# Optimization experiments

Measured on AMD Instinct MI355X. Metric: run time of the kernel, lower is better.

## Reference

```python
import jax, jax.numpy as jnp
import numpy as np
from jax import lax


def _viterbi_decode(logits, trans):
    """Batched Viterbi decode (tf.contrib.crf.crf_decode semantics, full lengths).
    logits: [B, T, U] unary potentials; trans: [U, U], trans[i, j] = score(i -> j).
    Returns int32 tags [B, T]."""
    logits_t = jnp.swapaxes(logits, 0, 1)  # [T, B, U]
    init_v = logits_t[0]                   # [B, U]

    def fwd_step(v, logit_t):
        # scores[b, i, j] = v[b, i] + trans[i, j]
        scores = v[:, :, None] + trans[None, :, :]          # [B, U, U]
        bp = jnp.argmax(scores, axis=1).astype(jnp.int32)   # [B, U] best prev tag
        v_new = jnp.max(scores, axis=1) + logit_t           # [B, U]
        return v_new, bp

    v_last, bps = lax.scan(fwd_step, init_v, logits_t[1:])  # bps: [T-1, B, U]
    last_tag = jnp.argmax(v_last, axis=1).astype(jnp.int32)  # [B]

    def bwd_step(tag, bp):
        # tag is the tag at t+1; bp[b, k] = best tag at t given tag k at t+1
        new_tag = jnp.take_along_axis(bp, tag[:, None], axis=1)[:, 0]
        return new_tag, new_tag

    _, tags_prefix = lax.scan(bwd_step, last_tag, bps, reverse=True)  # [T-1, B]
    tags = jnp.concatenate([tags_prefix, last_tag[None, :]], axis=0)  # [T, B]
    return jnp.swapaxes(tags, 0, 1)  # [B, T]


def setup_inputs() -> dict:
    key = jax.random.key(0)
    k0, k1, k2, k3, k4 = jax.random.split(key, 5)
    B, T, D, U = 64, 512, 1024, 128
    x = jax.random.normal(k0, (B, T, D), dtype=jnp.float32)
    kernel = jax.random.normal(k1, (D, U), dtype=jnp.float32) * (1.0 / np.sqrt(D))
    bias = jnp.zeros((U,), dtype=jnp.float32)
    chain_kernel = jax.random.normal(k2, (U, U), dtype=jnp.float32) * 0.1
    left_boundary = jax.random.normal(k3, (U,), dtype=jnp.float32) * 0.1
    right_boundary = jax.random.normal(k4, (U,), dtype=jnp.float32) * 0.1
    return {
        "x": x,
        "kernel": kernel,
        "bias": bias,
        "chain_kernel": chain_kernel,
        "left_boundary": left_boundary,
        "right_boundary": right_boundary,
    }


def reference(x, kernel, bias, chain_kernel, left_boundary, right_boundary):
    # _dense_layer: linear activation, x @ kernel + bias
    logits = jnp.einsum("btd,du->btu", x, kernel) + bias  # [B, T, U]
    # add_boundary_energy with mask=None: boundaries on first / last timestep
    logits = logits.at[:, 0, :].add(left_boundary)
    logits = logits.at[:, -1, :].add(right_boundary)
    # test_mode='viterbi', learn_mode='join': return decoded tags cast to float32
    tags = _viterbi_decode(logits, chain_kernel)
    return tags.astype(jnp.float32)
```

## Files before the change

kernel.cpp:

```cpp
#include <hip/hip_runtime.h>

#define T_SEQ 512
#define U_TAGS 128
#define D_DIM 1024
#define M_ROWS (64 * T_SEQ)

__global__ __launch_bounds__(256) void crf_gemm_half(
    const float* __restrict__ A, const float* __restrict__ Bk,
    float* __restrict__ Cpart) {
  __shared__ float As[16][132];
  __shared__ float Bs[16][132];
  const int tid = threadIdx.x;
  const int tx = tid & 15, ty = tid >> 4;
  const int row0 = blockIdx.x * 128;
  const int kbase = blockIdx.y * (D_DIM / 2);

  const int am = tid >> 2, ak = (tid & 3) << 2;
  const int bk = tid >> 5, bn = (tid & 31) << 2;

  float acc[8][8] = {};

  float4 a0 = *(const float4*)&A[(size_t)(row0 + am) * D_DIM + kbase + ak];
  float4 a1 = *(const float4*)&A[(size_t)(row0 + am + 64) * D_DIM + kbase + ak];
  float4 b0 = *(const float4*)&Bk[(size_t)(kbase + bk) * U_TAGS + bn];
  float4 b1 = *(const float4*)&Bk[(size_t)(kbase + bk + 8) * U_TAGS + bn];

  for (int k0 = 0; k0 < D_DIM / 2; k0 += 16) {
    As[ak + 0][am] = a0.x; As[ak + 1][am] = a0.y;
    As[ak + 2][am] = a0.z; As[ak + 3][am] = a0.w;
    As[ak + 0][am + 64] = a1.x; As[ak + 1][am + 64] = a1.y;
    As[ak + 2][am + 64] = a1.z; As[ak + 3][am + 64] = a1.w;
    *(float4*)&Bs[bk][bn] = b0;
    *(float4*)&Bs[bk + 8][bn] = b1;
    __syncthreads();
    if (k0 + 16 < D_DIM / 2) {
      const int kn = kbase + k0 + 16;
      a0 = *(const float4*)&A[(size_t)(row0 + am) * D_DIM + kn + ak];
      a1 = *(const float4*)&A[(size_t)(row0 + am + 64) * D_DIM + kn + ak];
      b0 = *(const float4*)&Bk[(size_t)(kn + bk) * U_TAGS + bn];
      b1 = *(const float4*)&Bk[(size_t)(kn + bk + 8) * U_TAGS + bn];
    }
#pragma unroll
    for (int kk = 0; kk < 16; ++kk) {
      float a[8], b[8];
      *(float4*)&a[0] = *(const float4*)&As[kk][ty * 8];
      *(float4*)&a[4] = *(const float4*)&As[kk][ty * 8 + 4];
      *(float4*)&b[0] = *(const float4*)&Bs[kk][tx * 4];
      *(float4*)&b[4] = *(const float4*)&Bs[kk][tx * 4 + 64];
#pragma unroll
      for (int r = 0; r < 8; ++r)
#pragma unroll
        for (int c = 0; c < 8; ++c) acc[r][c] = fmaf(a[r], b[c], acc[r][c]);
    }
    __syncthreads();
  }

  float* Cp = Cpart + (size_t)blockIdx.y * M_ROWS * U_TAGS;
#pragma unroll
  for (int r = 0; r < 8; ++r) {
    const int row = row0 + ty * 8 + r;
    *(float4*)&Cp[(size_t)row * U_TAGS + tx * 4] = *(float4*)&acc[r][0];
    *(float4*)&Cp[(size_t)row * U_TAGS + tx * 4 + 64] = *(float4*)&acc[r][4];
  }
}

__global__ __launch_bounds__(256) void crf_combine(
    float* __restrict__ p, const float* __restrict__ bias,
    const float* __restrict__ lb, const float* __restrict__ rb) {
  const int i = blockIdx.x * 256 + threadIdx.x;
  const int row = i >> 5;
  const int col = (i & 31) << 2;
  const int t = row & (T_SEQ - 1);
  const float* p1 = p + (size_t)M_ROWS * U_TAGS;
  float4 v0 = *(const float4*)&p[(size_t)i * 4];
  float4 v1 = *(const float4*)&p1[(size_t)i * 4];
  float4 bb = *(const float4*)&bias[col];
  float4 o;
  o.x = v0.x + v1.x + bb.x; o.y = v0.y + v1.y + bb.y;
  o.z = v0.z + v1.z + bb.z; o.w = v0.w + v1.w + bb.w;
  if (t == 0) {
    float4 l = *(const float4*)&lb[col];
    o.x += l.x; o.y += l.y; o.z += l.z; o.w += l.w;
  }
  if (t == T_SEQ - 1) {
    float4 r = *(const float4*)&rb[col];
    o.x += r.x; o.y += r.y; o.z += r.z; o.w += r.w;
  }
  *(float4*)&p[(size_t)i * 4] = o;
}

__global__ __launch_bounds__(256) void crf_gemm(
    const float* __restrict__ A, const float* __restrict__ Bk,
    const float* __restrict__ bias, const float* __restrict__ lb,
    const float* __restrict__ rb, float* __restrict__ C) {
  __shared__ float As[16][132];
  __shared__ float Bs[16][132];
  const int tid = threadIdx.x;
  const int tx = tid & 15, ty = tid >> 4;
  const int row0 = blockIdx.x * 128;
  const int am = tid >> 2, ak = (tid & 3) << 2;
  const int bk = tid >> 5, bn = (tid & 31) << 2;
  float acc[8][8] = {};
  float4 a0 = *(const float4*)&A[(size_t)(row0 + am) * D_DIM + ak];
  float4 a1 = *(const float4*)&A[(size_t)(row0 + am + 64) * D_DIM + ak];
  float4 b0 = *(const float4*)&Bk[(size_t)bk * U_TAGS + bn];
  float4 b1 = *(const float4*)&Bk[(size_t)(bk + 8) * U_TAGS + bn];
  for (int k0 = 0; k0 < D_DIM; k0 += 16) {
    As[ak + 0][am] = a0.x; As[ak + 1][am] = a0.y;
    As[ak + 2][am] = a0.z; As[ak + 3][am] = a0.w;
    As[ak + 0][am + 64] = a1.x; As[ak + 1][am + 64] = a1.y;
    As[ak + 2][am + 64] = a1.z; As[ak + 3][am + 64] = a1.w;
    *(float4*)&Bs[bk][bn] = b0;
    *(float4*)&Bs[bk + 8][bn] = b1;
    __syncthreads();
    if (k0 + 16 < D_DIM) {
      a0 = *(const float4*)&A[(size_t)(row0 + am) * D_DIM + k0 + 16 + ak];
      a1 = *(const float4*)&A[(size_t)(row0 + am + 64) * D_DIM + k0 + 16 + ak];
      b0 = *(const float4*)&Bk[(size_t)(k0 + 16 + bk) * U_TAGS + bn];
      b1 = *(const float4*)&Bk[(size_t)(k0 + 16 + bk + 8) * U_TAGS + bn];
    }
#pragma unroll
    for (int kk = 0; kk < 16; ++kk) {
      float a[8], b[8];
      *(float4*)&a[0] = *(const float4*)&As[kk][ty * 8];
      *(float4*)&a[4] = *(const float4*)&As[kk][ty * 8 + 4];
      *(float4*)&b[0] = *(const float4*)&Bs[kk][tx * 4];
      *(float4*)&b[4] = *(const float4*)&Bs[kk][tx * 4 + 64];
#pragma unroll
      for (int r = 0; r < 8; ++r)
#pragma unroll
        for (int c = 0; c < 8; ++c) acc[r][c] = fmaf(a[r], b[c], acc[r][c]);
    }
    __syncthreads();
  }
#pragma unroll
  for (int r = 0; r < 8; ++r) {
    const int row = row0 + ty * 8 + r;
    const int t = row & (T_SEQ - 1);
    const int n0 = tx * 4, n1 = tx * 4 + 64;
    float o[8];
#pragma unroll
    for (int c = 0; c < 4; ++c) {
      float v = acc[r][c] + bias[n0 + c];
      if (t == 0) v += lb[n0 + c];
      if (t == T_SEQ - 1) v += rb[n0 + c];
      o[c] = v;
    }
#pragma unroll
    for (int c = 0; c < 4; ++c) {
      float v = acc[r][c + 4] + bias[n1 + c];
      if (t == 0) v += lb[n1 + c];
      if (t == T_SEQ - 1) v += rb[n1 + c];
      o[c + 4] = v;
    }
    *(float4*)&C[(size_t)row * U_TAGS + n0] = *(float4*)&o[0];
    *(float4*)&C[(size_t)row * U_TAGS + n1] = *(float4*)&o[4];
  }
}

__device__ __forceinline__ float rl_f(float v, int lane) {
  return __int_as_float(__builtin_amdgcn_readlane(__float_as_int(v), lane));
}
template <int CTRL>
__device__ __forceinline__ float dpp_max_step(float x) {
  int v = __float_as_int(x);
  int t = __builtin_amdgcn_update_dpp(v, v, CTRL, 0xF, 0xF, false);
  return fmaxf(x, __int_as_float(t));
}
__device__ __forceinline__ float wave_max64_bcast(float x) {
  x = dpp_max_step<0x111>(x);
  x = dpp_max_step<0x112>(x);
  x = dpp_max_step<0x114>(x);
  x = dpp_max_step<0x118>(x);
  x = dpp_max_step<0x142>(x);
  x = dpp_max_step<0x143>(x);
  return rl_f(x, 63);
}
__device__ __forceinline__ void win(float sa, int ia, float sb, int ib,
                                    float& so, int& io) {
  bool g = sa >= sb;
  so = g ? sa : sb;
  io = g ? ia : ib;
}

__global__ __launch_bounds__(256) void crf_viterbi(
    const float* __restrict__ logits,
    const float* __restrict__ trans,
    float* __restrict__ out) {
  __shared__ __align__(16) float trs[U_TAGS * U_TAGS];
  __shared__ __align__(16) unsigned char bp[(T_SEQ - 1) * U_TAGS];
  __shared__ __align__(16) float ring[4 * 8 * U_TAGS];
  __shared__ int flags[2];
  __shared__ unsigned char tags[T_SEQ];
  __shared__ unsigned char M[8][U_TAGS];
  __shared__ unsigned char seedE[8];
  __shared__ float rmaxs[U_TAGS];
  __shared__ float wmin2[2];
  __shared__ float gminS;
  __shared__ int lastTagS;

  const int b = blockIdx.x;
  const int tid = threadIdx.x;
  const float* lg_b = logits + (size_t)b * T_SEQ * U_TAGS;

#pragma unroll
  for (int it = 0; it < 16; ++it)
    *(float4*)&trs[(it * 256 + tid) * 4] =
        *(const float4*)&trans[(it * 256 + tid) * 4];
  if (tid == 0) { flags[0] = 0; flags[1] = 0; }
  __syncthreads();

  float rowmin = 1e30f;
  if (tid < U_TAGS) {
    float mx = -1e30f, mn = 1e30f;
    for (int q = 0; q < 32; ++q) {
      float4 v = *(const float4*)&trs[tid * U_TAGS + q * 4];
      mx = fmaxf(fmaxf(mx, v.x), fmaxf(v.y, fmaxf(v.z, v.w)));
      mn = fminf(fminf(mn, v.x), fminf(v.y, fminf(v.z, v.w)));
    }
    rmaxs[tid] = mx;
    rowmin = mn;
#pragma unroll
    for (int off = 1; off < 64; off <<= 1)
      rowmin = fminf(rowmin, __shfl_xor(rowmin, off));
    if ((tid & 63) == 0) wmin2[tid >> 6] = rowmin;
  }
  __syncthreads();
  if (tid == 0) gminS = fminf(wmin2[0], wmin2[1]);
  __syncthreads();

  const int wv = tid >> 6, l = tid & 63;
  volatile int* vfl = (volatile int*)flags;

  if (wv == 1) {
    const float4* src = (const float4*)lg_b;
    float4* dst = (float4*)ring;
    for (int c = 0; c < 64; ++c) {
      while (vfl[1] + 4 <= c) { }
      const float4* s4 = src + c * 256;
      float4 d0 = s4[l], d1 = s4[l + 64], d2 = s4[l + 128], d3 = s4[l + 192];
      float4* d4 = dst + (c & 3) * 256;
      d4[l] = d0; d4[l + 64] = d1; d4[l + 128] = d2; d4[l + 192] = d3;
      __threadfence_block();
      if (l == 0) vfl[0] = c + 1;
    }
  } else if (wv == 0) {
    const float cc0 = rmaxs[l] - gminS + 0.01f;
    const float cc1 = rmaxs[64 + l] - gminS + 0.01f;
    while (vfl[0] < 1) { }
    float v0 = ring[l];
    float v1 = ring[64 + l];
    const unsigned long long G = 0x8000000000000000ull;
    int bpoff = l;

    for (int t = 1; t < T_SEQ; ++t) {
      if ((t & 7) == 0) {
        const int c = t >> 3;
        if (l == 0) vfl[1] = c;
        while (vfl[0] <= c) { }
      }
      const float* sl = ring + ((t >> 3) & 3) * 1024 + (t & 7) * U_TAGS;
      float lg0 = sl[l];
      float lg1 = sl[64 + l];

      const float vm = wave_max64_bcast(fmaxf(v0, v1));
      unsigned long long m0 = __ballot(v0 + cc0 >= vm);
      unsigned long long m1 = __ballot(v1 + cc1 >= vm);

      unsigned long long rA1 = m0 & (m0 - 1), rA2 = rA1 & (rA1 - 1);
      unsigned long long rB1 = m1 & (m1 - 1), rB2 = rB1 & (rB1 - 1);
      const int iA0 = __builtin_ctzll(m0 | G);
      const int iA1 = __builtin_ctzll(rA1 | G);
      const int iA2 = __builtin_ctzll(rA2 | G);
      const int iB0 = __builtin_ctzll(m1 | G);
      const int iB1 = __builtin_ctzll(rB1 | G);
      const int iB2 = __builtin_ctzll(rB2 | G);
      unsigned long long tail = (rA2 & (rA2 - 1)) | (rB2 & (rB2 - 1));

      const float svA0 = rl_f(v0, iA0), svA1 = rl_f(v0, iA1),
                  svA2 = rl_f(v0, iA2);
      const float svB0 = rl_f(v1, iB0), svB1 = rl_f(v1, iB1),
                  svB2 = rl_f(v1, iB2);

      const float* pA0 = &trs[iA0 * U_TAGS + l];
      const float* pA1 = &trs[iA1 * U_TAGS + l];
      const float* pA2 = &trs[iA2 * U_TAGS + l];
      const float* pB0 = &trs[(64 + iB0) * U_TAGS + l];
      const float* pB1 = &trs[(64 + iB1) * U_TAGS + l];
      const float* pB2 = &trs[(64 + iB2) * U_TAGS + l];
      const float tA0L = pA0[0], tA0H = pA0[64];
      const float tA1L = pA1[0], tA1H = pA1[64];
      const float tA2L = pA2[0], tA2H = pA2[64];
      const float tB0L = pB0[0], tB0H = pB0[64];
      const float tB1L = pB1[0], tB1H = pB1[64];
      const float tB2L = pB2[0], tB2H = pB2[64];

      float wa, wb, wL; int xa, xb, xL;
      win(svA0 + tA0L, iA0, svA1 + tA1L, iA1, wa, xa);
      win(wa, xa, svA2 + tA2L, iA2, wa, xa);
      win(svB0 + tB0L, 64 + iB0, svB1 + tB1L, 64 + iB1, wb, xb);
      win(wb, xb, svB2 + tB2L, 64 + iB2, wb, xb);
      win(wa, xa, wb, xb, wL, xL);
      float wH; int xH;
      win(svA0 + tA0H, iA0, svA1 + tA1H, iA1, wa, xa);
      win(wa, xa, svA2 + tA2H, iA2, wa, xa);
      win(svB0 + tB0H, 64 + iB0, svB1 + tB1H, 64 + iB1, wb, xb);
      win(wb, xb, svB2 + tB2H, 64 + iB2, wb, xb);
      win(wa, xa, wb, xb, wH, xH);

      if (tail) {
        unsigned long long r = rA2 & (rA2 - 1);
        while (r) {
          int i = __builtin_ctzll(r); r &= r - 1;
          float vi = rl_f(v0, i);
          float sL = vi + trs[i * U_TAGS + l];
          float sH = vi + trs[i * U_TAGS + 64 + l];
          if (sL > wL || (sL == wL && i < xL)) { wL = sL; xL = i; }
          if (sH > wH || (sH == wH && i < xH)) { wH = sH; xH = i; }
        }
        r = rB2 & (rB2 - 1);
        while (r) {
          int i = __builtin_ctzll(r); r &= r - 1;
          float vi = rl_f(v1, i);
          float sL = vi + trs[(64 + i) * U_TAGS + l];
          float sH = vi + trs[(64 + i) * U_TAGS + 64 + l];
          if (sL > wL || (sL == wL && 64 + i < xL)) { wL = sL; xL = 64 + i; }
          if (sH > wH || (sH == wH && 64 + i < xH)) { wH = sH; xH = 64 + i; }
        }
      }

      bp[bpoff] = (unsigned char)xL;
      bp[bpoff + 64] = (unsigned char)xH;
      bpoff += U_TAGS;
      v0 = wL + lg0;
      v1 = wH + lg1;
    }

    float val = v0; int idx = l;
    if (v1 > v0) { val = v1; idx = 64 + l; }
#pragma unroll
    for (int off = 1; off < 64; off <<= 1) {
      float vo = __shfl_xor(val, off);
      int io = __shfl_xor(idx, off);
      if (vo > val || (vo == val && io < idx)) { val = vo; idx = io; }
    }
    if (l == 0) { lastTagS = idx; tags[T_SEQ - 1] = (unsigned char)idx; }
  }
  __syncthreads();

#pragma unroll
  for (int q = 0; q < 4; ++q) {
    const int chain = tid + q * 256;
    const int c = chain >> 7, s = chain & 127;
    const int lo = c * 64;
    const int hi = (c == 7) ? (T_SEQ - 2) : (c * 64 + 63);
    int cur = s;
    for (int t = hi; t >= lo; --t) cur = bp[t * U_TAGS + cur];
    M[c][s] = (unsigned char)cur;
  }
  __syncthreads();
  if (tid == 0) {
    int e = lastTagS;
    seedE[7] = (unsigned char)e;
    for (int c = 7; c >= 1; --c) { e = M[c][e]; seedE[c - 1] = (unsigned char)e; }
  }
  __syncthreads();
  if (tid < 8) {
    const int c = tid;
    const int lo = c * 64;
    const int hi = (c == 7) ? (T_SEQ - 2) : (c * 64 + 63);
    int cur = seedE[c];
    for (int t = hi; t >= lo; --t) {
      cur = bp[t * U_TAGS + cur];
      tags[t] = (unsigned char)cur;
    }
  }
  __syncthreads();
  out[(size_t)b * T_SEQ + tid] = (float)tags[tid];
  out[(size_t)b * T_SEQ + 256 + tid] = (float)tags[256 + tid];
}

extern "C" void kernel_launch(void* const* d_in, const int* in_sizes, int n_in,
                              void* d_out, int out_size, void* d_ws,
                              size_t ws_size, hipStream_t stream) {
  const float* x = (const float*)d_in[0];
  const float* kern = (const float*)d_in[1];
  const float* bias = (const float*)d_in[2];
  const float* chain = (const float*)d_in[3];
  const float* lb = (const float*)d_in[4];
  const float* rb = (const float*)d_in[5];
  float* out = (float*)d_out;
  float* logits = (float*)d_ws;

  const size_t part = (size_t)M_ROWS * U_TAGS * sizeof(float);
  if (ws_size >= 2 * part) {
    crf_gemm_half<<<dim3(256, 2), 256, 0, stream>>>(x, kern, logits);
    crf_combine<<<(M_ROWS * U_TAGS / 4 + 255) / 256, 256, 0, stream>>>(
        logits, bias, lb, rb);
  } else {
    crf_gemm<<<256, 256, 0, stream>>>(x, kern, bias, lb, rb, logits);
  }
  crf_viterbi<<<64, 256, 0, stream>>>(logits, chain, out);
}
```

Baseline: 586.3 us.

## Fuse split-K combine into Viterbi loader and retile GEMM to 512 threads

The separate combine kernel, which summed the two split-K partial logits and added the bias and boundary terms, is removed. The Viterbi kernel's producer wave now reads both partials and does that sum while filling its shared-memory ring. This drops one kernel launch and a full read-modify-write pass over the logits. The split-K GEMM is also retiled to 512 threads with a 32-deep K step and a 4x8 per-thread tile, which lowers register pressure but gives each thread less reuse per loaded value. The cost is that the serial Viterbi producer wave now reads twice the data.

```diff
diff --git a/kernel.cpp b/kernel.cpp
--- a/kernel.cpp
+++ b/kernel.cpp
@@ -5,50 +5,51 @@
 #define D_DIM 1024
 #define M_ROWS (64 * T_SEQ)
 
-__global__ __launch_bounds__(256) void crf_gemm_half(
+__global__ __launch_bounds__(512) void crf_gemm_half(
     const float* __restrict__ A, const float* __restrict__ Bk,
     float* __restrict__ Cpart) {
-  __shared__ float As[16][132];
-  __shared__ float Bs[16][132];
+  __shared__ float As[32][132];
+  __shared__ float Bs[32][132];
   const int tid = threadIdx.x;
-  const int tx = tid & 15, ty = tid >> 4;
   const int row0 = blockIdx.x * 128;
   const int kbase = blockIdx.y * (D_DIM / 2);
 
-  const int am = tid >> 2, ak = (tid & 3) << 2;
-  const int bk = tid >> 5, bn = (tid & 31) << 2;
-
-  float acc[8][8] = {};
-
-  float4 a0 = *(const float4*)&A[(size_t)(row0 + am) * D_DIM + kbase + ak];
-  float4 a1 = *(const float4*)&A[(size_t)(row0 + am + 64) * D_DIM + kbase + ak];
-  float4 b0 = *(const float4*)&Bk[(size_t)(kbase + bk) * U_TAGS + bn];
-  float4 b1 = *(const float4*)&Bk[(size_t)(kbase + bk + 8) * U_TAGS + bn];
-
-  for (int k0 = 0; k0 < D_DIM / 2; k0 += 16) {
-    As[ak + 0][am] = a0.x; As[ak + 1][am] = a0.y;
-    As[ak + 2][am] = a0.z; As[ak + 3][am] = a0.w;
-    As[ak + 0][am + 64] = a1.x; As[ak + 1][am + 64] = a1.y;
-    As[ak + 2][am + 64] = a1.z; As[ak + 3][am + 64] = a1.w;
-    *(float4*)&Bs[bk][bn] = b0;
-    *(float4*)&Bs[bk + 8][bn] = b1;
+  const int tx = tid & 15, ty = tid >> 4;
+
+  const int ar = tid >> 3, aq = tid & 7;
+  const int bk = tid >> 5, bn = tid & 31;
+
+  float acc[4][8] = {};
+
+  float4 a0 = *(const float4*)&A[(size_t)(row0 + ar) * D_DIM + kbase + aq * 4];
+  float4 a1 =
+      *(const float4*)&A[(size_t)(row0 + ar + 64) * D_DIM + kbase + aq * 4];
+  float4 b0 = *(const float4*)&Bk[(size_t)(kbase + bk) * U_TAGS + bn * 4];
+  float4 b1 = *(const float4*)&Bk[(size_t)(kbase + bk + 16) * U_TAGS + bn * 4];
+
+  for (int k0 = 0; k0 < D_DIM / 2; k0 += 32) {
+    As[aq * 4 + 0][ar] = a0.x; As[aq * 4 + 1][ar] = a0.y;
+    As[aq * 4 + 2][ar] = a0.z; As[aq * 4 + 3][ar] = a0.w;
+    As[aq * 4 + 0][ar + 64] = a1.x; As[aq * 4 + 1][ar + 64] = a1.y;
+    As[aq * 4 + 2][ar + 64] = a1.z; As[aq * 4 + 3][ar + 64] = a1.w;
+    *(float4*)&Bs[bk][bn * 4] = b0;
+    *(float4*)&Bs[bk + 16][bn * 4] = b1;
     __syncthreads();
-    if (k0 + 16 < D_DIM / 2) {
-      const int kn = kbase + k0 + 16;
-      a0 = *(const float4*)&A[(size_t)(row0 + am) * D_DIM + kn + ak];
-      a1 = *(const float4*)&A[(size_t)(row0 + am + 64) * D_DIM + kn + ak];
-      b0 = *(const float4*)&Bk[(size_t)(kn + bk) * U_TAGS + bn];
-      b1 = *(const float4*)&Bk[(size_t)(kn + bk + 8) * U_TAGS + bn];
-    }
-#pragma unroll
-    for (int kk = 0; kk < 16; ++kk) {
-      float a[8], b[8];
-      *(float4*)&a[0] = *(const float4*)&As[kk][ty * 8];
-      *(float4*)&a[4] = *(const float4*)&As[kk][ty * 8 + 4];
+    if (k0 + 32 < D_DIM / 2) {
+      const int kn = kbase + k0 + 32;
+      a0 = *(const float4*)&A[(size_t)(row0 + ar) * D_DIM + kn + aq * 4];
+      a1 = *(const float4*)&A[(size_t)(row0 + ar + 64) * D_DIM + kn + aq * 4];
+      b0 = *(const float4*)&Bk[(size_t)(kn + bk) * U_TAGS + bn * 4];
+      b1 = *(const float4*)&Bk[(size_t)(kn + bk + 16) * U_TAGS + bn * 4];
+    }
+#pragma unroll
+    for (int kk = 0; kk < 32; ++kk) {
+      float a[4], b[8];
+      *(float4*)&a[0] = *(const float4*)&As[kk][ty * 4];
       *(float4*)&b[0] = *(const float4*)&Bs[kk][tx * 4];
       *(float4*)&b[4] = *(const float4*)&Bs[kk][tx * 4 + 64];
 #pragma unroll
-      for (int r = 0; r < 8; ++r)
+      for (int r = 0; r < 4; ++r)
 #pragma unroll
         for (int c = 0; c < 8; ++c) acc[r][c] = fmaf(a[r], b[c], acc[r][c]);
     }
@@ -57,36 +58,11 @@
 
   float* Cp = Cpart + (size_t)blockIdx.y * M_ROWS * U_TAGS;
 #pragma unroll
-  for (int r = 0; r < 8; ++r) {
-    const int row = row0 + ty * 8 + r;
+  for (int r = 0; r < 4; ++r) {
+    const int row = row0 + ty * 4 + r;
     *(float4*)&Cp[(size_t)row * U_TAGS + tx * 4] = *(float4*)&acc[r][0];
     *(float4*)&Cp[(size_t)row * U_TAGS + tx * 4 + 64] = *(float4*)&acc[r][4];
   }
-}
-
-__global__ __launch_bounds__(256) void crf_combine(
-    float* __restrict__ p, const float* __restrict__ bias,
-    const float* __restrict__ lb, const float* __restrict__ rb) {
-  const int i = blockIdx.x * 256 + threadIdx.x;
-  const int row = i >> 5;
-  const int col = (i & 31) << 2;
-  const int t = row & (T_SEQ - 1);
-  const float* p1 = p + (size_t)M_ROWS * U_TAGS;
-  float4 v0 = *(const float4*)&p[(size_t)i * 4];
-  float4 v1 = *(const float4*)&p1[(size_t)i * 4];
-  float4 bb = *(const float4*)&bias[col];
-  float4 o;
-  o.x = v0.x + v1.x + bb.x; o.y = v0.y + v1.y + bb.y;
-  o.z = v0.z + v1.z + bb.z; o.w = v0.w + v1.w + bb.w;
-  if (t == 0) {
-    float4 l = *(const float4*)&lb[col];
-    o.x += l.x; o.y += l.y; o.z += l.z; o.w += l.w;
-  }
-  if (t == T_SEQ - 1) {
-    float4 r = *(const float4*)&rb[col];
-    o.x += r.x; o.y += r.y; o.z += r.z; o.w += r.w;
-  }
-  *(float4*)&p[(size_t)i * 4] = o;
 }
 
 __global__ __launch_bounds__(256) void crf_gemm(
@@ -183,8 +159,10 @@
   io = g ? ia : ib;
 }
 
-__global__ __launch_bounds__(256) void crf_viterbi(
-    const float* __restrict__ logits,
+__global__ __launch_bounds__(256) void crf_viterbi_fc(
+    const float* __restrict__ ws,
+    const float* __restrict__ bias, const float* __restrict__ lb,
+    const float* __restrict__ rb,
     const float* __restrict__ trans,
     float* __restrict__ out) {
   __shared__ __align__(16) float trs[U_TAGS * U_TAGS];
@@ -201,7 +179,6 @@
 
   const int b = blockIdx.x;
   const int tid = threadIdx.x;
-  const float* lg_b = logits + (size_t)b * T_SEQ * U_TAGS;
 
 #pragma unroll
   for (int it = 0; it < 16; ++it)
@@ -233,14 +210,37 @@
   volatile int* vfl = (volatile int*)flags;
 
   if (wv == 1) {
-    const float4* src = (const float4*)lg_b;
+    const float4* p04 = (const float4*)ws + (size_t)b * 16384;
+    const float4* p14 =
+        (const float4*)(ws + (size_t)M_ROWS * U_TAGS) + (size_t)b * 16384;
+    const float4 bias4 = ((const float4*)bias)[l & 31];
+    const float4 lb4 = ((const float4*)lb)[l & 31];
+    const float4 rb4 = ((const float4*)rb)[l & 31];
     float4* dst = (float4*)ring;
     for (int c = 0; c < 64; ++c) {
       while (vfl[1] + 4 <= c) { }
-      const float4* s4 = src + c * 256;
-      float4 d0 = s4[l], d1 = s4[l + 64], d2 = s4[l + 128], d3 = s4[l + 192];
+      const int i0 = c * 256 + l;
+      float4 v[4];
+#pragma unroll
+      for (int u = 0; u < 4; ++u) {
+        const int f4g = i0 + u * 64;
+        const float4 x0 = p04[f4g];
+        const float4 x1 = p14[f4g];
+        float4 o;
+        o.x = x0.x + x1.x + bias4.x;
+        o.y = x0.y + x1.y + bias4.y;
+        o.z = x0.z + x1.z + bias4.z;
+        o.w = x0.w + x1.w + bias4.w;
+        if (f4g < 32) {
+          o.x += lb4.x; o.y += lb4.y; o.z += lb4.z; o.w += lb4.w;
+        }
+        if (f4g >= 32 * (T_SEQ - 1)) {
+          o.x += rb4.x; o.y += rb4.y; o.z += rb4.z; o.w += rb4.w;
+        }
+        v[u] = o;
+      }
       float4* d4 = dst + (c & 3) * 256;
-      d4[l] = d0; d4[l + 64] = d1; d4[l + 128] = d2; d4[l + 192] = d3;
+      d4[l] = v[0]; d4[l + 64] = v[1]; d4[l + 128] = v[2]; d4[l + 192] = v[3];
       __threadfence_block();
       if (l == 0) vfl[0] = c + 1;
     }
@@ -380,6 +380,202 @@
   out[(size_t)b * T_SEQ + 256 + tid] = (float)tags[256 + tid];
 }
 
+__global__ __launch_bounds__(256) void crf_viterbi(
+    const float* __restrict__ logits, const float* __restrict__ trans,
+    float* __restrict__ out) {
+  __shared__ __align__(16) float trs[U_TAGS * U_TAGS];
+  __shared__ __align__(16) unsigned char bp[(T_SEQ - 1) * U_TAGS];
+  __shared__ __align__(16) float ring[4 * 8 * U_TAGS];
+  __shared__ int flags[2];
+  __shared__ unsigned char tags[T_SEQ];
+  __shared__ unsigned char M[8][U_TAGS];
+  __shared__ unsigned char seedE[8];
+  __shared__ float rmaxs[U_TAGS];
+  __shared__ float wmin2[2];
+  __shared__ float gminS;
+  __shared__ int lastTagS;
+
+  const int b = blockIdx.x;
+  const int tid = threadIdx.x;
+  const float* lg_b = logits + (size_t)b * T_SEQ * U_TAGS;
+
+#pragma unroll
+  for (int it = 0; it < 16; ++it)
+    *(float4*)&trs[(it * 256 + tid) * 4] =
+        *(const float4*)&trans[(it * 256 + tid) * 4];
+  if (tid == 0) { flags[0] = 0; flags[1] = 0; }
+  __syncthreads();
+
+  float rowmin = 1e30f;
+  if (tid < U_TAGS) {
+    float mx = -1e30f, mn = 1e30f;
+    for (int q = 0; q < 32; ++q) {
+      float4 v = *(const float4*)&trs[tid * U_TAGS + q * 4];
+      mx = fmaxf(fmaxf(mx, v.x), fmaxf(v.y, fmaxf(v.z, v.w)));
+      mn = fminf(fminf(mn, v.x), fminf(v.y, fminf(v.z, v.w)));
+    }
+    rmaxs[tid] = mx;
+    rowmin = mn;
+#pragma unroll
+    for (int off = 1; off < 64; off <<= 1)
+      rowmin = fminf(rowmin, __shfl_xor(rowmin, off));
+    if ((tid & 63) == 0) wmin2[tid >> 6] = rowmin;
+  }
+  __syncthreads();
+  if (tid == 0) gminS = fminf(wmin2[0], wmin2[1]);
+  __syncthreads();
+
+  const int wv = tid >> 6, l = tid & 63;
+  volatile int* vfl = (volatile int*)flags;
+
+  if (wv == 1) {
+    const float4* src = (const float4*)lg_b;
+    float4* dst = (float4*)ring;
+    for (int c = 0; c < 64; ++c) {
+      while (vfl[1] + 4 <= c) { }
+      const float4* s4 = src + c * 256;
+      float4 d0 = s4[l], d1 = s4[l + 64], d2 = s4[l + 128], d3 = s4[l + 192];
+      float4* d4 = dst + (c & 3) * 256;
+      d4[l] = d0; d4[l + 64] = d1; d4[l + 128] = d2; d4[l + 192] = d3;
+      __threadfence_block();
+      if (l == 0) vfl[0] = c + 1;
+    }
+  } else if (wv == 0) {
+    const float cc0 = rmaxs[l] - gminS + 0.01f;
+    const float cc1 = rmaxs[64 + l] - gminS + 0.01f;
+    while (vfl[0] < 1) { }
+    float v0 = ring[l];
+    float v1 = ring[64 + l];
+    const unsigned long long G = 0x8000000000000000ull;
+    int bpoff = l;
+
+    for (int t = 1; t < T_SEQ; ++t) {
+      if ((t & 7) == 0) {
+        const int c = t >> 3;
+        if (l == 0) vfl[1] = c;
+        while (vfl[0] <= c) { }
+      }
+      const float* sl = ring + ((t >> 3) & 3) * 1024 + (t & 7) * U_TAGS;
+      float lg0 = sl[l];
+      float lg1 = sl[64 + l];
+
+      const float vm = wave_max64_bcast(fmaxf(v0, v1));
+      unsigned long long m0 = __ballot(v0 + cc0 >= vm);
+      unsigned long long m1 = __ballot(v1 + cc1 >= vm);
+
+      unsigned long long rA1 = m0 & (m0 - 1), rA2 = rA1 & (rA1 - 1);
+      unsigned long long rB1 = m1 & (m1 - 1), rB2 = rB1 & (rB1 - 1);
+      const int iA0 = __builtin_ctzll(m0 | G);
+      const int iA1 = __builtin_ctzll(rA1 | G);
+      const int iA2 = __builtin_ctzll(rA2 | G);
+      const int iB0 = __builtin_ctzll(m1 | G);
+      const int iB1 = __builtin_ctzll(rB1 | G);
+      const int iB2 = __builtin_ctzll(rB2 | G);
+      unsigned long long tail = (rA2 & (rA2 - 1)) | (rB2 & (rB2 - 1));
+
+      const float svA0 = rl_f(v0, iA0), svA1 = rl_f(v0, iA1),
+                  svA2 = rl_f(v0, iA2);
+      const float svB0 = rl_f(v1, iB0), svB1 = rl_f(v1, iB1),
+                  svB2 = rl_f(v1, iB2);
+
+      const float* pA0 = &trs[iA0 * U_TAGS + l];
+      const float* pA1 = &trs[iA1 * U_TAGS + l];
+      const float* pA2 = &trs[iA2 * U_TAGS + l];
+      const float* pB0 = &trs[(64 + iB0) * U_TAGS + l];
+      const float* pB1 = &trs[(64 + iB1) * U_TAGS + l];
+      const float* pB2 = &trs[(64 + iB2) * U_TAGS + l];
+      const float tA0L = pA0[0], tA0H = pA0[64];
+      const float tA1L = pA1[0], tA1H = pA1[64];
+      const float tA2L = pA2[0], tA2H = pA2[64];
+      const float tB0L = pB0[0], tB0H = pB0[64];
+      const float tB1L = pB1[0], tB1H = pB1[64];
+      const float tB2L = pB2[0], tB2H = pB2[64];
+
+      float wa, wb, wL; int xa, xb, xL;
+      win(svA0 + tA0L, iA0, svA1 + tA1L, iA1, wa, xa);
+      win(wa, xa, svA2 + tA2L, iA2, wa, xa);
+      win(svB0 + tB0L, 64 + iB0, svB1 + tB1L, 64 + iB1, wb, xb);
+      win(wb, xb, svB2 + tB2L, 64 + iB2, wb, xb);
+      win(wa, xa, wb, xb, wL, xL);
+      float wH; int xH;
+      win(svA0 + tA0H, iA0, svA1 + tA1H, iA1, wa, xa);
+      win(wa, xa, svA2 + tA2H, iA2, wa, xa);
+      win(svB0 + tB0H, 64 + iB0, svB1 + tB1H, 64 + iB1, wb, xb);
+      win(wb, xb, svB2 + tB2H, 64 + iB2, wb, xb);
+      win(wa, xa, wb, xb, wH, xH);
+
+      if (tail) {
+        unsigned long long r = rA2 & (rA2 - 1);
+        while (r) {
+          int i = __builtin_ctzll(r); r &= r - 1;
+          float vi = rl_f(v0, i);
+          float sL = vi + trs[i * U_TAGS + l];
+          float sH = vi + trs[i * U_TAGS + 64 + l];
+          if (sL > wL || (sL == wL && i < xL)) { wL = sL; xL = i; }
+          if (sH > wH || (sH == wH && i < xH)) { wH = sH; xH = i; }
+        }
+        r = rB2 & (rB2 - 1);
+        while (r) {
+          int i = __builtin_ctzll(r); r &= r - 1;
+          float vi = rl_f(v1, i);
+          float sL = vi + trs[(64 + i) * U_TAGS + l];
+          float sH = vi + trs[(64 + i) * U_TAGS + 64 + l];
+          if (sL > wL || (sL == wL && 64 + i < xL)) { wL = sL; xL = 64 + i; }
+          if (sH > wH || (sH == wH && 64 + i < xH)) { wH = sH; xH = 64 + i; }
+        }
+      }
+
+      bp[bpoff] = (unsigned char)xL;
+      bp[bpoff + 64] = (unsigned char)xH;
+      bpoff += U_TAGS;
+      v0 = wL + lg0;
+      v1 = wH + lg1;
+    }
+
+    float val = v0; int idx = l;
+    if (v1 > v0) { val = v1; idx = 64 + l; }
+#pragma unroll
+    for (int off = 1; off < 64; off <<= 1) {
+      float vo = __shfl_xor(val, off);
+      int io = __shfl_xor(idx, off);
+      if (vo > val || (vo == val && io < idx)) { val = vo; idx = io; }
+    }
+    if (l == 0) { lastTagS = idx; tags[T_SEQ - 1] = (unsigned char)idx; }
+  }
+  __syncthreads();
+
+#pragma unroll
+  for (int q = 0; q < 4; ++q) {
+    const int chain = tid + q * 256;
+    const int c = chain >> 7, s = chain & 127;
+    const int lo = c * 64;
+    const int hi = (c == 7) ? (T_SEQ - 2) : (c * 64 + 63);
+    int cur = s;
+    for (int t = hi; t >= lo; --t) cur = bp[t * U_TAGS + cur];
+    M[c][s] = (unsigned char)cur;
+  }
+  __syncthreads();
+  if (tid == 0) {
+    int e = lastTagS;
+    seedE[7] = (unsigned char)e;
+    for (int c = 7; c >= 1; --c) { e = M[c][e]; seedE[c - 1] = (unsigned char)e; }
+  }
+  __syncthreads();
+  if (tid < 8) {
+    const int c = tid;
+    const int lo = c * 64;
+    const int hi = (c == 7) ? (T_SEQ - 2) : (c * 64 + 63);
+    int cur = seedE[c];
+    for (int t = hi; t >= lo; --t) {
+      cur = bp[t * U_TAGS + cur];
+      tags[t] = (unsigned char)cur;
+    }
+  }
+  __syncthreads();
+  out[(size_t)b * T_SEQ + tid] = (float)tags[tid];
+  out[(size_t)b * T_SEQ + 256 + tid] = (float)tags[256 + tid];
+}
+
 extern "C" void kernel_launch(void* const* d_in, const int* in_sizes, int n_in,
                               void* d_out, int out_size, void* d_ws,
                               size_t ws_size, hipStream_t stream) {
@@ -390,15 +586,15 @@
   const float* lb = (const float*)d_in[4];
   const float* rb = (const float*)d_in[5];
   float* out = (float*)d_out;
-  float* logits = (float*)d_ws;
 
   const size_t part = (size_t)M_ROWS * U_TAGS * sizeof(float);
   if (ws_size >= 2 * part) {
-    crf_gemm_half<<<dim3(256, 2), 256, 0, stream>>>(x, kern, logits);
-    crf_combine<<<(M_ROWS * U_TAGS / 4 + 255) / 256, 256, 0, stream>>>(
-        logits, bias, lb, rb);
+    crf_gemm_half<<<dim3(256, 2), 512, 0, stream>>>(x, kern, (float*)d_ws);
+    crf_viterbi_fc<<<64, 256, 0, stream>>>((const float*)d_ws, bias, lb, rb,
+                                           chain, out);
   } else {
+    float* logits = (float*)d_ws;
     crf_gemm<<<256, 256, 0, stream>>>(x, kern, bias, lb, rb, logits);
-  }
-  crf_viterbi<<<64, 256, 0, stream>>>(logits, chain, out);
-}
+    crf_viterbi<<<64, 256, 0, stream>>>(logits, chain, out);
+  }
+}
```

Result: no change. 588.8 us (+0.4%).
